# Optimization experiments

Hardware: AMD Instinct MI355X
Metric: run time of the kernel (lower is better)

## Reference

```python
import jax, jax.numpy as jnp
import numpy as np

B, H, S, D = 8, 16, 1024, 64

def setup_inputs() -> dict:
    key = jax.random.key(0)
    kq, kk, kv, km = jax.random.split(key, 4)
    Q = jax.random.normal(kq, (B, H, S, D), dtype=jnp.float32)
    K = jax.random.normal(kk, (B, H, S, D), dtype=jnp.float32)
    V = jax.random.normal(kv, (B, H, S, D), dtype=jnp.float32)
    attn_mask = jax.random.randint(km, (B, H, S, S), 0, 2).astype(bool)
    return {"Q": Q, "K": K, "V": V, "attn_mask": attn_mask}

def reference(Q, K, V, attn_mask):
    # scores = Q @ K^T  (NOTE: source has no 1/sqrt(d) scaling)
    scores = jnp.einsum("bhqd,bhkd->bhqk", Q, K)
    # source uses masked_fill_(mask, 1e-9), i.e. masked positions become 1e-9 (not -inf)
    scores = jnp.where(attn_mask, jnp.float32(1e-9), scores)
    attn = jax.nn.softmax(scores, axis=-1)
    context = jnp.einsum("bhqk,bhkd->bhqd", attn, V)
    return context, attn
```

## Files before the change

kernel.cpp:

```cpp
#include <hip/hip_runtime.h>

#define Sn 1024
#define Dn 64
#define PH_LD 1032
#define K_LD 72
#define V_LD 72

typedef short v8s __attribute__((ext_vector_type(8)));
typedef unsigned short v8u __attribute__((ext_vector_type(8)));
typedef float v4f __attribute__((ext_vector_type(4)));
typedef int   v4i __attribute__((ext_vector_type(4)));

#define LGKM0()  asm volatile("s_waitcnt lgkmcnt(0)" ::: "memory")
#define SBAR()   do { asm volatile("" ::: "memory"); __builtin_amdgcn_s_barrier(); \
                      __builtin_amdgcn_sched_barrier(0); } while (0)

__device__ __forceinline__ unsigned short f2bf(float x) {
    union { float f; unsigned u; } v; v.f = x;
    return (unsigned short)((v.u + 0x7FFFu + ((v.u >> 16) & 1u)) >> 16);
}
__device__ __forceinline__ float bf2f(unsigned short h) {
    union { float f; unsigned u; } v; v.u = ((unsigned)h) << 16;
    return v.f;
}
__device__ __forceinline__ void split2(float x, unsigned short& h, unsigned short& l) {
    unsigned short hs = f2bf(x);
    h = hs; l = f2bf(x - bf2f(hs));
}

__global__ __launch_bounds__(256) void prep_kf(const float* __restrict__ K,
    unsigned short* __restrict__ KF)
{
    const int bh = blockIdx.x >> 4, kt = blockIdx.x & 15;
    const int t = threadIdx.x;
    const int w = t >> 6, lane = t & 63;
    const int fr = lane & 15, g = lane >> 4;
    const float* src = K + (((size_t)(bh << 10) + (kt << 6) + (w << 4) + fr) << 6);
    const v4f a0 = __builtin_nontemporal_load((const v4f*)(src + (g << 3)));
    const v4f a1 = __builtin_nontemporal_load((const v4f*)(src + (g << 3) + 4));
    const v4f b0 = __builtin_nontemporal_load((const v4f*)(src + 32 + (g << 3)));
    const v4f b1 = __builtin_nontemporal_load((const v4f*)(src + 32 + (g << 3) + 4));
    v8u h0, h1, l0, l1;
    #pragma unroll
    for (int j = 0; j < 4; ++j) {
        unsigned short hh, ll;
        split2(a0[j], hh, ll); h0[j] = hh;     l0[j] = ll;
        split2(a1[j], hh, ll); h0[4 + j] = hh; l0[4 + j] = ll;
        split2(b0[j], hh, ll); h1[j] = hh;     l1[j] = ll;
        split2(b1[j], hh, ll); h1[4 + j] = hh; l1[4 + j] = ll;
    }
    unsigned short* dst = KF + ((size_t)bh << 17) + ((size_t)((kt << 2) + w) << 11) + (lane << 3);
    *(v8u*)(dst)        = h0;
    *(v8u*)(dst + 512)  = h1;
    *(v8u*)(dst + 1024) = l0;
    *(v8u*)(dst + 1536) = l1;
}

__global__ __launch_bounds__(256) void prep_vf(const float* __restrict__ V,
    unsigned short* __restrict__ VF)
{
    __shared__ float Ts[64][65];
    const int bh = blockIdx.x >> 4, kt = blockIdx.x & 15;
    const int t = threadIdx.x;
    {
        const int r = t >> 2, cs = (t & 3) << 4;
        const float* src = V + ((size_t)bh * Sn + (kt << 6) + r) * Dn + cs;
        const v4f a = __builtin_nontemporal_load((const v4f*)src);
        const v4f b = __builtin_nontemporal_load((const v4f*)src + 1);
        const v4f c = __builtin_nontemporal_load((const v4f*)src + 2);
        const v4f d = __builtin_nontemporal_load((const v4f*)src + 3);
        #pragma unroll
        for (int j = 0; j < 4; ++j) {
            Ts[r][cs + j]      = a[j];
            Ts[r][cs + 4 + j]  = b[j];
            Ts[r][cs + 8 + j]  = c[j];
            Ts[r][cs + 12 + j] = d[j];
        }
    }
    __syncthreads();
    {
        const int w = t >> 6, lane = t & 63;
        const int fr = lane & 15, g = lane >> 4;
        const int d = (w << 4) + fr;
        unsigned short* dst = VF + ((size_t)bh << 16) + ((size_t)((kt << 2) + w) << 10) + (lane << 3);
        v8u o0, o1;
        #pragma unroll
        for (int j = 0; j < 8; ++j) o0[j] = f2bf(Ts[(g << 3) + j][d]);
        #pragma unroll
        for (int j = 0; j < 8; ++j) o1[j] = f2bf(Ts[32 + (g << 3) + j][d]);
        *(v8u*)dst         = o0;
        *(v8u*)(dst + 512) = o1;
    }
}

__global__ __launch_bounds__(256) void prep_m(const int* __restrict__ M,
    unsigned long long* __restrict__ MW)
{
    const int NW = 2097152;
    const int lane = threadIdx.x & 63;
    const int wave = (blockIdx.x << 2) + (threadIdx.x >> 6);
    const int nwaves = gridDim.x << 2;
    for (int w0 = wave << 3; w0 < NW; w0 += nwaves << 3) {
        unsigned long long b[8];
        #pragma unroll
        for (int s = 0; s < 8; ++s) {
            const int v = __builtin_nontemporal_load(&M[((size_t)(w0 + s) << 6) + lane]);
            b[s] = __ballot(v != 0);
        }
        if (lane == 0) {
            ulonglong2* dst = (ulonglong2*)(MW + w0);
            ulonglong2 p0, p1, p2, p3;
            p0.x = b[0]; p0.y = b[1]; p1.x = b[2]; p1.y = b[3];
            p2.x = b[4]; p2.y = b[5]; p3.x = b[6]; p3.y = b[7];
            dst[0] = p0; dst[1] = p1; dst[2] = p2; dst[3] = p3;
        }
    }
}

__global__ __launch_bounds__(256, 4) void fused_attn_c(
    const unsigned short* __restrict__ KFG, const unsigned short* __restrict__ VFG,
    const float* __restrict__ Q, const unsigned long long* __restrict__ MW,
    float* __restrict__ attnO, float* __restrict__ ctxO)
{
    __shared__ unsigned short Ph[16][PH_LD];
    __shared__ float rsumW[4][16];
    __shared__ float invL[16];

    const int tid  = threadIdx.x;
    const int lane = tid & 63;
    const int w    = tid >> 6;
    const int fr   = lane & 15;
    const int g    = lane >> 4;

    const int swz = ((blockIdx.x & 7) << 10) + (blockIdx.x >> 3);
    const int bh = swz >> 6;
    const int q0 = (swz & 63) << 4;

    const float* Qb = Q + (size_t)bh * Sn * Dn + (size_t)q0 * Dn;
    float*       Ab = attnO + (size_t)bh * Sn * Sn + (size_t)q0 * Sn;
    float*       Cb = ctxO  + (size_t)bh * Sn * Dn + (size_t)q0 * Dn;
    const unsigned short* KFb = KFG + ((size_t)bh << 17);
    const unsigned short* VFb = VFG + ((size_t)bh << 16);
    const unsigned long long* mwp = MW + ((size_t)bh << 14) + ((size_t)(q0 + fr) << 4);

    v8s qh0, qh1, ql0, ql1;
    {
        const float* qp = Qb + fr * Dn + (g << 3);
        float x0[8], x1[8];
        *(v4f*)&x0[0] = *(const v4f*)qp;
        *(v4f*)&x0[4] = *(const v4f*)(qp + 4);
        *(v4f*)&x1[0] = *(const v4f*)(qp + 32);
        *(v4f*)&x1[4] = *(const v4f*)(qp + 36);
        #pragma unroll
        for (int i = 0; i < 8; ++i) {
            unsigned short hh, ll;
            split2(x0[i], hh, ll); qh0[i] = (short)hh; ql0[i] = (short)ll;
            split2(x1[i], hh, ll); qh1[i] = (short)hh; ql1[i] = (short)ll;
        }
    }

    const int sh = (w << 4) + (g << 2);

#define LDK(kt, h0, h1, l0, l1) do {                                               \
        const unsigned short* _p = KFb + ((size_t)(((kt) << 2) + w) << 11) + (lane << 3); \
        h0 = *(const v8s*)_p;          h1 = *(const v8s*)(_p + 512);               \
        l0 = *(const v8s*)(_p + 1024); l1 = *(const v8s*)(_p + 1536);              \
    } while (0)

#define STEPA(h0, h1, l0, l1, mwv, kt) do {                                        \
        v4f acc = {0.f, 0.f, 0.f, 0.f};                                            \
        __builtin_amdgcn_s_setprio(1);                                             \
        acc = __builtin_amdgcn_mfma_f32_16x16x32_bf16(h0, qh0, acc, 0, 0, 0);      \
        acc = __builtin_amdgcn_mfma_f32_16x16x32_bf16(h1, qh1, acc, 0, 0, 0);      \
        acc = __builtin_amdgcn_mfma_f32_16x16x32_bf16(l0, qh0, acc, 0, 0, 0);      \
        acc = __builtin_amdgcn_mfma_f32_16x16x32_bf16(l1, qh1, acc, 0, 0, 0);      \
        acc = __builtin_amdgcn_mfma_f32_16x16x32_bf16(h0, ql0, acc, 0, 0, 0);      \
        acc = __builtin_amdgcn_mfma_f32_16x16x32_bf16(h1, ql1, acc, 0, 0, 0);      \
        __builtin_amdgcn_s_setprio(0);                                             \
        const unsigned mb = (unsigned)((mwv) >> sh);                               \
        const float e0 = (mb & 1u) ? 1.0f : __expf(acc[0]);                        \
        const float e1 = (mb & 2u) ? 1.0f : __expf(acc[1]);                        \
        const float e2 = (mb & 4u) ? 1.0f : __expf(acc[2]);                        \
        const float e3 = (mb & 8u) ? 1.0f : __expf(acc[3]);                        \
        rs += (e0 + e1) + (e2 + e3);                                               \
        ushort4 pk;                                                                \
        pk.x = f2bf(e0); pk.y = f2bf(e1); pk.z = f2bf(e2); pk.w = f2bf(e3);        \
        *(ushort4*)&Ph[fr][((kt) << 6) + (w << 4) + (g << 2)] = pk;                \
    } while (0)

    float rs = 0.f;

    {
        v8s ah0, ah1, al0, al1, bh0, bh1, bl0, bl1;
        LDK(0, ah0, ah1, al0, al1);
        LDK(1, bh0, bh1, bl0, bl1);
        unsigned long long mA = mwp[0], mB = mwp[1];
        for (int kt = 0; kt < 16; kt += 2) {
            const int k2 = (kt + 2 < 16) ? kt + 2 : kt;
            const int k3 = (kt + 3 < 16) ? kt + 3 : kt;
            v8s ch0, ch1, cl0, cl1, dh0, dh1, dl0, dl1;
            LDK(k2, ch0, ch1, cl0, cl1);
            LDK(k3, dh0, dh1, dl0, dl1);
            const unsigned long long mC = mwp[k2];
            const unsigned long long mD = mwp[k3];
            STEPA(ah0, ah1, al0, al1, mA, kt);
            STEPA(bh0, bh1, bl0, bl1, mB, kt + 1);
            ah0 = ch0; ah1 = ch1; al0 = cl0; al1 = cl1; mA = mC;
            bh0 = dh0; bh1 = dh1; bl0 = dl0; bl1 = dl1; mB = mD;
        }
    }

    rs += __shfl_xor(rs, 16);
    rs += __shfl_xor(rs, 32);
    if (g == 0) rsumW[w][fr] = rs;
    __builtin_amdgcn_sched_barrier(0);
    LGKM0();
    SBAR();
    if (tid < 16) {
        const float s = rsumW[0][tid] + rsumW[1][tid] + rsumW[2][tid] + rsumW[3][tid];
        invL[tid] = 1.0f / s;
    }
    __builtin_amdgcn_sched_barrier(0);
    LGKM0();
    SBAR();

#define LDV(kt, v0, v1) do {                                                       \
        const unsigned short* _p = VFb + ((size_t)(((kt) << 2) + w) << 10) + (lane << 3); \
        v0 = *(const v8s*)_p;  v1 = *(const v8s*)(_p + 512);                       \
    } while (0)

#define STEPB(v0, v1, kt) do {                                                     \
        const v8s a0 = *(const v8s*)&Ph[fr][((kt) << 6) + (g << 3)];               \
        const v8s a1 = *(const v8s*)&Ph[fr][((kt) << 6) + 32 + (g << 3)];          \
        __builtin_amdgcn_s_setprio(1);                                             \
        accp = __builtin_amdgcn_mfma_f32_16x16x32_bf16(a0, v0, accp, 0, 0, 0);     \
        accp = __builtin_amdgcn_mfma_f32_16x16x32_bf16(a1, v1, accp, 0, 0, 0);     \
        __builtin_amdgcn_s_setprio(0);                                             \
    } while (0)

    v8s va0, va1, vb0, vb1;
    LDV(0, va0, va1);
    LDV(1, vb0, vb1);

    {
        const int qq = tid >> 4, ii = tid & 15;
        const float inv = invL[qq];
        float* arow = Ab + (size_t)qq * Sn;
        #pragma unroll
        for (int c = 0; c < 16; ++c) {
            const int k0 = (c << 6) + (ii << 2);
            const ushort4 p = *(const ushort4*)&Ph[qq][k0];
            v4f o;
            o[0] = bf2f(p.x) * inv; o[1] = bf2f(p.y) * inv;
            o[2] = bf2f(p.z) * inv; o[3] = bf2f(p.w) * inv;
            __builtin_nontemporal_store(o, (v4f*)(arow + k0));
        }
    }

    const int dcol = (w << 4) + fr;
    v4f accp = {0.f, 0.f, 0.f, 0.f};
    for (int kt = 0; kt < 16; kt += 2) {
        const int k2 = (kt + 2 < 16) ? kt + 2 : kt;
        const int k3 = (kt + 3 < 16) ? kt + 3 : kt;
        v8s vc0, vc1, vd0, vd1;
        LDV(k2, vc0, vc1);
        LDV(k3, vd0, vd1);
        STEPB(va0, va1, kt);
        STEPB(vb0, vb1, kt + 1);
        va0 = vc0; va1 = vc1;
        vb0 = vd0; vb1 = vd1;
    }
    #pragma unroll
    for (int r = 0; r < 4; ++r) {
        const int q = (g << 2) + r;
        __builtin_nontemporal_store(accp[r] * invL[q], &Cb[(size_t)q * Dn + dcol]);
    }
#undef LDK
#undef STEPA
#undef LDV
#undef STEPB
}

__global__ __launch_bounds__(256, 3) void fused_attn_fb(
    const float* __restrict__ Q, const float* __restrict__ K,
    const float* __restrict__ V, const int* __restrict__ M,
    float* __restrict__ attnO, float* __restrict__ ctxO)
{
    __shared__ unsigned short Ph[16][1048];
    __shared__ __align__(16) unsigned short Kraw[2 * 64 * K_LD];
    __shared__ float rsumW[4][16];
    __shared__ float invL[16];

    unsigned short (*Khi)[K_LD] = (unsigned short (*)[K_LD])Kraw;
    unsigned short (*Klo)[K_LD] = (unsigned short (*)[K_LD])(Kraw + 64 * K_LD);
    unsigned short (*Vt)[V_LD]  = (unsigned short (*)[V_LD])Kraw;

    const int tid  = threadIdx.x;
    const int lane = tid & 63;
    const int w    = tid >> 6;
    const int fr   = lane & 15;
    const int g    = lane >> 4;

    const int bh = blockIdx.x >> 6;
    const int q0 = (blockIdx.x & 63) << 4;

    const float* Qb = Q + (size_t)bh * Sn * Dn + (size_t)q0 * Dn;
    const float* Kb = K + (size_t)bh * Sn * Dn;
    const float* Vb = V + (size_t)bh * Sn * Dn;
    const int*   Mb = M + (size_t)bh * Sn * Sn + (size_t)q0 * Sn;
    float*       Ab = attnO + (size_t)bh * Sn * Sn + (size_t)q0 * Sn;
    float*       Cb = ctxO  + (size_t)bh * Sn * Dn + (size_t)q0 * Dn;

    v8s qh0, qh1, ql0, ql1;
    {
        const float* qp = Qb + fr * Dn + (g << 3);
        float x0[8], x1[8];
        *(v4f*)&x0[0] = *(const v4f*)qp;
        *(v4f*)&x0[4] = *(const v4f*)(qp + 4);
        *(v4f*)&x1[0] = *(const v4f*)(qp + 32);
        *(v4f*)&x1[4] = *(const v4f*)(qp + 36);
        #pragma unroll
        for (int i = 0; i < 8; ++i) {
            unsigned short hh, ll;
            split2(x0[i], hh, ll); qh0[i] = (short)hh; ql0[i] = (short)ll;
            split2(x1[i], hh, ll); qh1[i] = (short)hh; ql1[i] = (short)ll;
        }
    }

    const int srow = tid >> 4;
    const int sc4  = (tid & 15) << 2;

    const int* mp = Mb + (size_t)fr * Sn + (w << 4) + (g << 2);
    v4i mv = *(const v4i*)mp;

    v4f ka[4];
    #pragma unroll
    for (int i = 0; i < 4; ++i)
        ka[i] = *(const v4f*)(Kb + (size_t)(srow + (i << 4)) * Dn + sc4);

    float rs = 0.f;

    for (int kt = 0; kt < 16; ++kt) {
        __syncthreads();
        v4f kb[4];
        if (kt < 15) {
            const float* kn = Kb + (size_t)((kt + 1) << 6) * Dn;
            #pragma unroll
            for (int i = 0; i < 4; ++i)
                kb[i] = *(const v4f*)(kn + (size_t)(srow + (i << 4)) * Dn + sc4);
        }
        v4i mnext = mv;
        if (kt < 15) mnext = *(const v4i*)(mp + ((kt + 1) << 6));

        #pragma unroll
        for (int i = 0; i < 4; ++i) {
            const int row = srow + (i << 4);
            ushort4 hv, lv;
            split2(ka[i][0], hv.x, lv.x); split2(ka[i][1], hv.y, lv.y);
            split2(ka[i][2], hv.z, lv.z); split2(ka[i][3], hv.w, lv.w);
            *(ushort4*)&Khi[row][sc4] = hv;
            *(ushort4*)&Klo[row][sc4] = lv;
        }
        __syncthreads();

        const int krow = (w << 4) + fr;
        const v8s kh0 = *(const v8s*)&Khi[krow][(g << 3)];
        const v8s kh1 = *(const v8s*)&Khi[krow][32 + (g << 3)];
        const v8s kl0 = *(const v8s*)&Klo[krow][(g << 3)];
        const v8s kl1 = *(const v8s*)&Klo[krow][32 + (g << 3)];

        v4f acc = {0.f, 0.f, 0.f, 0.f};
        acc = __builtin_amdgcn_mfma_f32_16x16x32_bf16(kh0, qh0, acc, 0, 0, 0);
        acc = __builtin_amdgcn_mfma_f32_16x16x32_bf16(kh1, qh1, acc, 0, 0, 0);
        acc = __builtin_amdgcn_mfma_f32_16x16x32_bf16(kl0, qh0, acc, 0, 0, 0);
        acc = __builtin_amdgcn_mfma_f32_16x16x32_bf16(kl1, qh1, acc, 0, 0, 0);
        acc = __builtin_amdgcn_mfma_f32_16x16x32_bf16(kh0, ql0, acc, 0, 0, 0);
        acc = __builtin_amdgcn_mfma_f32_16x16x32_bf16(kh1, ql1, acc, 0, 0, 0);

        const float e0 = mv[0] ? 1.0f : __expf(acc[0]);
        const float e1 = mv[1] ? 1.0f : __expf(acc[1]);
        const float e2 = mv[2] ? 1.0f : __expf(acc[2]);
        const float e3 = mv[3] ? 1.0f : __expf(acc[3]);
        rs += (e0 + e1) + (e2 + e3);
        ushort4 pk;
        pk.x = f2bf(e0); pk.y = f2bf(e1); pk.z = f2bf(e2); pk.w = f2bf(e3);
        *(ushort4*)&Ph[fr][(kt << 6) + (w << 4) + (g << 2)] = pk;

        mv = mnext;
        #pragma unroll
        for (int i = 0; i < 4; ++i) ka[i] = kb[i];
    }

    rs += __shfl_xor(rs, 16);
    rs += __shfl_xor(rs, 32);
    if (g == 0) rsumW[w][fr] = rs;
    __syncthreads();
    if (tid < 16) {
        const float s = rsumW[0][tid] + rsumW[1][tid] + rsumW[2][tid] + rsumW[3][tid];
        invL[tid] = 1.0f / s;
    }
    __syncthreads();

    const int dcol = (w << 4) + fr;
    v4f va[4];
    #pragma unroll
    for (int i = 0; i < 4; ++i)
        va[i] = *(const v4f*)(Vb + (size_t)(srow + (i << 4)) * Dn + sc4);

    v4f accp = {0.f, 0.f, 0.f, 0.f};
    for (int kt = 0; kt < 16; ++kt) {
        __syncthreads();
        v4f vb[4];
        if (kt < 15) {
            const float* vn = Vb + (size_t)((kt + 1) << 6) * Dn;
            #pragma unroll
            for (int i = 0; i < 4; ++i)
                vb[i] = *(const v4f*)(vn + (size_t)(srow + (i << 4)) * Dn + sc4);
        }
        #pragma unroll
        for (int i = 0; i < 4; ++i) {
            const int row = srow + (i << 4);
            Vt[sc4 + 0][row] = f2bf(va[i][0]);
            Vt[sc4 + 1][row] = f2bf(va[i][1]);
            Vt[sc4 + 2][row] = f2bf(va[i][2]);
            Vt[sc4 + 3][row] = f2bf(va[i][3]);
        }
        __syncthreads();

        #pragma unroll
        for (int c = 0; c < 2; ++c) {
            const int kc = (kt << 6) + (c << 5);
            const v8s a = *(const v8s*)&Ph[fr][kc + (g << 3)];
            const v8s b = *(const v8s*)&Vt[dcol][(c << 5) + (g << 3)];
            accp = __builtin_amdgcn_mfma_f32_16x16x32_bf16(a, b, accp, 0, 0, 0);
        }
        #pragma unroll
        for (int i = 0; i < 4; ++i) va[i] = vb[i];
    }
    #pragma unroll
    for (int r = 0; r < 4; ++r) {
        const int q = (g << 2) + r;
        Cb[(size_t)q * Dn + dcol] = accp[r] * invL[q];
    }

    {
        const int qq = tid >> 4, ii = tid & 15;
        const float inv = invL[qq];
        float* arow = Ab + (size_t)qq * Sn;
        #pragma unroll
        for (int c = 0; c < 16; ++c) {
            const int k0 = (c << 6) + (ii << 2);
            const ushort4 p = *(const ushort4*)&Ph[qq][k0];
            v4f o;
            o[0] = bf2f(p.x) * inv; o[1] = bf2f(p.y) * inv;
            o[2] = bf2f(p.z) * inv; o[3] = bf2f(p.w) * inv;
            *(v4f*)(arow + k0) = o;
        }
    }
}

extern "C" void kernel_launch(void* const* d_in, const int* in_sizes, int n_in,
                              void* d_out, int out_size, void* d_ws, size_t ws_size,
                              hipStream_t stream) {
    const float* Q    = (const float*)d_in[0];
    const float* K    = (const float*)d_in[1];
    const float* V    = (const float*)d_in[2];
    const int*   mask = (const int*)d_in[3];

    float* ctx  = (float*)d_out;
    float* attn = (float*)d_out + (size_t)128 * Sn * Dn;

    const size_t NELEM = (size_t)128 * Sn * Dn;
    const size_t MWORDS = (size_t)128 * Sn * 16;
    const size_t NEED  = NELEM * 2 * 3 + MWORDS * 8;

    if (ws_size >= NEED) {
        unsigned short* KF = (unsigned short*)d_ws;
        unsigned short* VF = KF + NELEM * 2;
        unsigned long long* MWp = (unsigned long long*)((char*)d_ws + NELEM * 2 * 3);
        prep_kf<<<2048, 256, 0, stream>>>(K, KF);
        prep_vf<<<2048, 256, 0, stream>>>(V, VF);
        prep_m<<<2048, 256, 0, stream>>>(mask, MWp);
        fused_attn_c<<<128 * 64, 256, 0, stream>>>(KF, VF, Q, MWp, attn, ctx);
    } else {
        fused_attn_fb<<<128 * 64, 256, 0, stream>>>(Q, K, V, mask, attn, ctx);
    }
}
```

Before: 293.3 us.

## Drop mask bit-packing prep kernel and read int mask directly in fused kernel

Removes the separate prep_m kernel that packed the int32 mask into 64-bit bitmasks. The fused attention kernel now loads int32 mask values directly with 16-byte vector loads, prefetching up to eight steps ahead in a register ring. The K-fragment double buffer becomes an array-indexed, fully unrolled loop. This saves one kernel launch and the write and re-read of the packed mask, but the main kernel now reads 32x more mask bytes and uses more registers, which may reduce occupancy.

```diff
diff --git a/kernel.cpp b/kernel.cpp
--- a/kernel.cpp
+++ b/kernel.cpp
@@ -93,33 +93,9 @@
     }
 }
 
-__global__ __launch_bounds__(256) void prep_m(const int* __restrict__ M,
-    unsigned long long* __restrict__ MW)
-{
-    const int NW = 2097152;
-    const int lane = threadIdx.x & 63;
-    const int wave = (blockIdx.x << 2) + (threadIdx.x >> 6);
-    const int nwaves = gridDim.x << 2;
-    for (int w0 = wave << 3; w0 < NW; w0 += nwaves << 3) {
-        unsigned long long b[8];
-        #pragma unroll
-        for (int s = 0; s < 8; ++s) {
-            const int v = __builtin_nontemporal_load(&M[((size_t)(w0 + s) << 6) + lane]);
-            b[s] = __ballot(v != 0);
-        }
-        if (lane == 0) {
-            ulonglong2* dst = (ulonglong2*)(MW + w0);
-            ulonglong2 p0, p1, p2, p3;
-            p0.x = b[0]; p0.y = b[1]; p1.x = b[2]; p1.y = b[3];
-            p2.x = b[4]; p2.y = b[5]; p3.x = b[6]; p3.y = b[7];
-            dst[0] = p0; dst[1] = p1; dst[2] = p2; dst[3] = p3;
-        }
-    }
-}
-
 __global__ __launch_bounds__(256, 4) void fused_attn_c(
     const unsigned short* __restrict__ KFG, const unsigned short* __restrict__ VFG,
-    const float* __restrict__ Q, const unsigned long long* __restrict__ MW,
+    const float* __restrict__ Q, const int* __restrict__ M,
     float* __restrict__ attnO, float* __restrict__ ctxO)
 {
     __shared__ unsigned short Ph[16][PH_LD];
@@ -141,7 +117,7 @@
     float*       Cb = ctxO  + (size_t)bh * Sn * Dn + (size_t)q0 * Dn;
     const unsigned short* KFb = KFG + ((size_t)bh << 17);
     const unsigned short* VFb = VFG + ((size_t)bh << 16);
-    const unsigned long long* mwp = MW + ((size_t)bh << 14) + ((size_t)(q0 + fr) << 4);
+    const int* mp = M + (size_t)bh * Sn * Sn + (size_t)(q0 + fr) * Sn + (w << 4) + (g << 2);
 
     v8s qh0, qh1, ql0, ql1;
     {
@@ -159,15 +135,13 @@
         }
     }
 
-    const int sh = (w << 4) + (g << 2);
-
 #define LDK(kt, h0, h1, l0, l1) do {                                               \
         const unsigned short* _p = KFb + ((size_t)(((kt) << 2) + w) << 11) + (lane << 3); \
         h0 = *(const v8s*)_p;          h1 = *(const v8s*)(_p + 512);               \
         l0 = *(const v8s*)(_p + 1024); l1 = *(const v8s*)(_p + 1536);              \
     } while (0)
 
-#define STEPA(h0, h1, l0, l1, mwv, kt) do {                                        \
+#define STEPA(h0, h1, l0, l1, mv, kt) do {                                         \
         v4f acc = {0.f, 0.f, 0.f, 0.f};                                            \
         __builtin_amdgcn_s_setprio(1);                                             \
         acc = __builtin_amdgcn_mfma_f32_16x16x32_bf16(h0, qh0, acc, 0, 0, 0);      \
@@ -177,11 +151,10 @@
         acc = __builtin_amdgcn_mfma_f32_16x16x32_bf16(h0, ql0, acc, 0, 0, 0);      \
         acc = __builtin_amdgcn_mfma_f32_16x16x32_bf16(h1, ql1, acc, 0, 0, 0);      \
         __builtin_amdgcn_s_setprio(0);                                             \
-        const unsigned mb = (unsigned)((mwv) >> sh);                               \
-        const float e0 = (mb & 1u) ? 1.0f : __expf(acc[0]);                        \
-        const float e1 = (mb & 2u) ? 1.0f : __expf(acc[1]);                        \
-        const float e2 = (mb & 4u) ? 1.0f : __expf(acc[2]);                        \
-        const float e3 = (mb & 8u) ? 1.0f : __expf(acc[3]);                        \
+        const float e0 = (mv)[0] ? 1.0f : __expf(acc[0]);                          \
+        const float e1 = (mv)[1] ? 1.0f : __expf(acc[1]);                          \
+        const float e2 = (mv)[2] ? 1.0f : __expf(acc[2]);                          \
+        const float e3 = (mv)[3] ? 1.0f : __expf(acc[3]);                          \
         rs += (e0 + e1) + (e2 + e3);                                               \
         ushort4 pk;                                                                \
         pk.x = f2bf(e0); pk.y = f2bf(e1); pk.z = f2bf(e2); pk.w = f2bf(e3);        \
@@ -191,22 +164,17 @@
     float rs = 0.f;
 
     {
-        v8s ah0, ah1, al0, al1, bh0, bh1, bl0, bl1;
-        LDK(0, ah0, ah1, al0, al1);
-        LDK(1, bh0, bh1, bl0, bl1);
-        unsigned long long mA = mwp[0], mB = mwp[1];
-        for (int kt = 0; kt < 16; kt += 2) {
-            const int k2 = (kt + 2 < 16) ? kt + 2 : kt;
-            const int k3 = (kt + 3 < 16) ? kt + 3 : kt;
-            v8s ch0, ch1, cl0, cl1, dh0, dh1, dl0, dl1;
-            LDK(k2, ch0, ch1, cl0, cl1);
-            LDK(k3, dh0, dh1, dl0, dl1);
-            const unsigned long long mC = mwp[k2];
-            const unsigned long long mD = mwp[k3];
-            STEPA(ah0, ah1, al0, al1, mA, kt);
-            STEPA(bh0, bh1, bl0, bl1, mB, kt + 1);
-            ah0 = ch0; ah1 = ch1; al0 = cl0; al1 = cl1; mA = mC;
-            bh0 = dh0; bh1 = dh1; bl0 = dl0; bl1 = dl1; mB = mD;
+        v8s h0[2], h1[2], l0[2], l1[2];
+        v4i mk[8];
+        LDK(0, h0[0], h1[0], l0[0], l1[0]);
+        LDK(1, h0[1], h1[1], l0[1], l1[1]);
+        #pragma unroll
+        for (int s = 0; s < 8; ++s) mk[s] = *(const v4i*)(mp + (s << 6));
+        #pragma unroll
+        for (int kt = 0; kt < 16; ++kt) {
+            STEPA(h0[kt & 1], h1[kt & 1], l0[kt & 1], l1[kt & 1], mk[kt & 7], kt);
+            if (kt + 2 < 16) LDK(kt + 2, h0[kt & 1], h1[kt & 1], l0[kt & 1], l1[kt & 1]);
+            if (kt + 8 < 16) mk[kt & 7] = *(const v4i*)(mp + ((kt + 8) << 6));
         }
     }
 
@@ -471,17 +439,14 @@
     float* attn = (float*)d_out + (size_t)128 * Sn * Dn;
 
     const size_t NELEM = (size_t)128 * Sn * Dn;
-    const size_t MWORDS = (size_t)128 * Sn * 16;
-    const size_t NEED  = NELEM * 2 * 3 + MWORDS * 8;
+    const size_t NEED  = NELEM * 6;
 
     if (ws_size >= NEED) {
         unsigned short* KF = (unsigned short*)d_ws;
         unsigned short* VF = KF + NELEM * 2;
-        unsigned long long* MWp = (unsigned long long*)((char*)d_ws + NELEM * 2 * 3);
         prep_kf<<<2048, 256, 0, stream>>>(K, KF);
         prep_vf<<<2048, 256, 0, stream>>>(V, VF);
-        prep_m<<<2048, 256, 0, stream>>>(mask, MWp);
-        fused_attn_c<<<128 * 64, 256, 0, stream>>>(KF, VF, Q, MWp, attn, ctx);
+        fused_attn_c<<<128 * 64, 256, 0, stream>>>(KF, VF, Q, mask, attn, ctx);
     } else {
         fused_attn_fb<<<128 * 64, 256, 0, stream>>>(Q, K, V, mask, attn, ctx);
     }
```

New measurement: 373.1 us. 27.2% more time.

## Process 32 query rows per 512-thread block to share K fragments

Applied to the files above, without the earlier changes.

Each block now covers 32 query rows with 8 waves instead of 16 rows with 4. In the QK^T phase every wave computes two 16-row query tiles against each loaded K tile, so K and mask traffic per query is halved, with a double-buffered prefetch loop. The PV phase splits the waves into two query halves and four D columns, and the grid shrinks to match. The shared P buffer doubles in size, which limits blocks per CU. The launch bound of 512 threads with 4 blocks per CU may cap registers and cause spills with the doubled query fragments.

```diff
diff --git a/kernel.cpp b/kernel.cpp
--- a/kernel.cpp
+++ b/kernel.cpp
@@ -117,14 +117,14 @@
     }
 }
 
-__global__ __launch_bounds__(256, 4) void fused_attn_c(
+__global__ __launch_bounds__(512, 4) void fused_attn_w(
     const unsigned short* __restrict__ KFG, const unsigned short* __restrict__ VFG,
     const float* __restrict__ Q, const unsigned long long* __restrict__ MW,
     float* __restrict__ attnO, float* __restrict__ ctxO)
 {
-    __shared__ unsigned short Ph[16][PH_LD];
-    __shared__ float rsumW[4][16];
-    __shared__ float invL[16];
+    __shared__ unsigned short Ph[32][PH_LD];
+    __shared__ float rsumW[8][32];
+    __shared__ float invL[32];
 
     const int tid  = threadIdx.x;
     const int lane = tid & 63;
@@ -132,20 +132,22 @@
     const int fr   = lane & 15;
     const int g    = lane >> 4;
 
-    const int swz = ((blockIdx.x & 7) << 10) + (blockIdx.x >> 3);
-    const int bh = swz >> 6;
-    const int q0 = (swz & 63) << 4;
+    const int swz = ((blockIdx.x & 7) << 9) + (blockIdx.x >> 3);
+    const int bh = swz >> 5;
+    const int q0 = (swz & 31) << 5;
 
     const float* Qb = Q + (size_t)bh * Sn * Dn + (size_t)q0 * Dn;
     float*       Ab = attnO + (size_t)bh * Sn * Sn + (size_t)q0 * Sn;
     float*       Cb = ctxO  + (size_t)bh * Sn * Dn + (size_t)q0 * Dn;
     const unsigned short* KFb = KFG + ((size_t)bh << 17);
     const unsigned short* VFb = VFG + ((size_t)bh << 16);
-    const unsigned long long* mwp = MW + ((size_t)bh << 14) + ((size_t)(q0 + fr) << 4);
-
-    v8s qh0, qh1, ql0, ql1;
-    {
-        const float* qp = Qb + fr * Dn + (g << 3);
+    const unsigned long long* mwp0 = MW + ((size_t)bh << 14) + ((size_t)(q0 + fr) << 4);
+    const unsigned long long* mwp1 = mwp0 + (16 << 4);
+
+    v8s qh0[2], qh1[2], ql0[2], ql1[2];
+    #pragma unroll
+    for (int h = 0; h < 2; ++h) {
+        const float* qp = Qb + (size_t)((h << 4) + fr) * Dn + (g << 3);
         float x0[8], x1[8];
         *(v4f*)&x0[0] = *(const v4f*)qp;
         *(v4f*)&x0[4] = *(const v4f*)(qp + 4);
@@ -154,70 +156,90 @@
         #pragma unroll
         for (int i = 0; i < 8; ++i) {
             unsigned short hh, ll;
-            split2(x0[i], hh, ll); qh0[i] = (short)hh; ql0[i] = (short)ll;
-            split2(x1[i], hh, ll); qh1[i] = (short)hh; ql1[i] = (short)ll;
-        }
-    }
-
-    const int sh = (w << 4) + (g << 2);
-
-#define LDK(kt, h0, h1, l0, l1) do {                                               \
-        const unsigned short* _p = KFb + ((size_t)(((kt) << 2) + w) << 11) + (lane << 3); \
-        h0 = *(const v8s*)_p;          h1 = *(const v8s*)(_p + 512);               \
-        l0 = *(const v8s*)(_p + 1024); l1 = *(const v8s*)(_p + 1536);              \
+            split2(x0[i], hh, ll); qh0[h][i] = (short)hh; ql0[h][i] = (short)ll;
+            split2(x1[i], hh, ll); qh1[h][i] = (short)hh; ql1[h][i] = (short)ll;
+        }
+    }
+
+    const int jbase = w >> 2;
+    const int sh    = ((w & 3) << 4) + (g << 2);
+
+#define LDK(kt, h0_, h1_, l0_, l1_) do {                                           \
+        const unsigned short* _p = KFb + ((size_t)(((kt) << 3) + w) << 11) + (lane << 3); \
+        h0_ = *(const v8s*)_p;          h1_ = *(const v8s*)(_p + 512);             \
+        l0_ = *(const v8s*)(_p + 1024); l1_ = *(const v8s*)(_p + 1536);            \
     } while (0)
 
-#define STEPA(h0, h1, l0, l1, mwv, kt) do {                                        \
-        v4f acc = {0.f, 0.f, 0.f, 0.f};                                            \
+#define STEPA(kh0, kh1, kl0, kl1, mv0, mv1, kt) do {                               \
+        v4f acc0 = {0.f, 0.f, 0.f, 0.f};                                           \
+        v4f acc1 = {0.f, 0.f, 0.f, 0.f};                                           \
         __builtin_amdgcn_s_setprio(1);                                             \
-        acc = __builtin_amdgcn_mfma_f32_16x16x32_bf16(h0, qh0, acc, 0, 0, 0);      \
-        acc = __builtin_amdgcn_mfma_f32_16x16x32_bf16(h1, qh1, acc, 0, 0, 0);      \
-        acc = __builtin_amdgcn_mfma_f32_16x16x32_bf16(l0, qh0, acc, 0, 0, 0);      \
-        acc = __builtin_amdgcn_mfma_f32_16x16x32_bf16(l1, qh1, acc, 0, 0, 0);      \
-        acc = __builtin_amdgcn_mfma_f32_16x16x32_bf16(h0, ql0, acc, 0, 0, 0);      \
-        acc = __builtin_amdgcn_mfma_f32_16x16x32_bf16(h1, ql1, acc, 0, 0, 0);      \
+        acc0 = __builtin_amdgcn_mfma_f32_16x16x32_bf16(kh0, qh0[0], acc0, 0, 0, 0);\
+        acc1 = __builtin_amdgcn_mfma_f32_16x16x32_bf16(kh0, qh0[1], acc1, 0, 0, 0);\
+        acc0 = __builtin_amdgcn_mfma_f32_16x16x32_bf16(kh1, qh1[0], acc0, 0, 0, 0);\
+        acc1 = __builtin_amdgcn_mfma_f32_16x16x32_bf16(kh1, qh1[1], acc1, 0, 0, 0);\
+        acc0 = __builtin_amdgcn_mfma_f32_16x16x32_bf16(kl0, qh0[0], acc0, 0, 0, 0);\
+        acc1 = __builtin_amdgcn_mfma_f32_16x16x32_bf16(kl0, qh0[1], acc1, 0, 0, 0);\
+        acc0 = __builtin_amdgcn_mfma_f32_16x16x32_bf16(kl1, qh1[0], acc0, 0, 0, 0);\
+        acc1 = __builtin_amdgcn_mfma_f32_16x16x32_bf16(kl1, qh1[1], acc1, 0, 0, 0);\
+        acc0 = __builtin_amdgcn_mfma_f32_16x16x32_bf16(kh0, ql0[0], acc0, 0, 0, 0);\
+        acc1 = __builtin_amdgcn_mfma_f32_16x16x32_bf16(kh0, ql0[1], acc1, 0, 0, 0);\
+        acc0 = __builtin_amdgcn_mfma_f32_16x16x32_bf16(kh1, ql1[0], acc0, 0, 0, 0);\
+        acc1 = __builtin_amdgcn_mfma_f32_16x16x32_bf16(kh1, ql1[1], acc1, 0, 0, 0);\
         __builtin_amdgcn_s_setprio(0);                                             \
-        const unsigned mb = (unsigned)((mwv) >> sh);                               \
-        const float e0 = (mb & 1u) ? 1.0f : __expf(acc[0]);                        \
-        const float e1 = (mb & 2u) ? 1.0f : __expf(acc[1]);                        \
-        const float e2 = (mb & 4u) ? 1.0f : __expf(acc[2]);                        \
-        const float e3 = (mb & 8u) ? 1.0f : __expf(acc[3]);                        \
-        rs += (e0 + e1) + (e2 + e3);                                               \
-        ushort4 pk;                                                                \
-        pk.x = f2bf(e0); pk.y = f2bf(e1); pk.z = f2bf(e2); pk.w = f2bf(e3);        \
-        *(ushort4*)&Ph[fr][((kt) << 6) + (w << 4) + (g << 2)] = pk;                \
+        const int kcol = ((kt) << 7) + ((w & 3) << 4) + ((w >> 2) << 6) + (g << 2);\
+        const unsigned mb0 = (unsigned)((mv0) >> sh);                              \
+        const unsigned mb1 = (unsigned)((mv1) >> sh);                              \
+        const float e00 = (mb0 & 1u) ? 1.0f : __expf(acc0[0]);                     \
+        const float e01 = (mb0 & 2u) ? 1.0f : __expf(acc0[1]);                     \
+        const float e02 = (mb0 & 4u) ? 1.0f : __expf(acc0[2]);                     \
+        const float e03 = (mb0 & 8u) ? 1.0f : __expf(acc0[3]);                     \
+        const float e10 = (mb1 & 1u) ? 1.0f : __expf(acc1[0]);                     \
+        const float e11 = (mb1 & 2u) ? 1.0f : __expf(acc1[1]);                     \
+        const float e12 = (mb1 & 4u) ? 1.0f : __expf(acc1[2]);                     \
+        const float e13 = (mb1 & 8u) ? 1.0f : __expf(acc1[3]);                     \
+        rs0 += (e00 + e01) + (e02 + e03);                                          \
+        rs1 += (e10 + e11) + (e12 + e13);                                          \
+        ushort4 pk0, pk1;                                                          \
+        pk0.x = f2bf(e00); pk0.y = f2bf(e01); pk0.z = f2bf(e02); pk0.w = f2bf(e03);\
+        pk1.x = f2bf(e10); pk1.y = f2bf(e11); pk1.z = f2bf(e12); pk1.w = f2bf(e13);\
+        *(ushort4*)&Ph[fr][kcol]      = pk0;                                       \
+        *(ushort4*)&Ph[16 + fr][kcol] = pk1;                                       \
     } while (0)
 
-    float rs = 0.f;
+    float rs0 = 0.f, rs1 = 0.f;
 
     {
-        v8s ah0, ah1, al0, al1, bh0, bh1, bl0, bl1;
-        LDK(0, ah0, ah1, al0, al1);
-        LDK(1, bh0, bh1, bl0, bl1);
-        unsigned long long mA = mwp[0], mB = mwp[1];
-        for (int kt = 0; kt < 16; kt += 2) {
-            const int k2 = (kt + 2 < 16) ? kt + 2 : kt;
-            const int k3 = (kt + 3 < 16) ? kt + 3 : kt;
-            v8s ch0, ch1, cl0, cl1, dh0, dh1, dl0, dl1;
-            LDK(k2, ch0, ch1, cl0, cl1);
-            LDK(k3, dh0, dh1, dl0, dl1);
-            const unsigned long long mC = mwp[k2];
-            const unsigned long long mD = mwp[k3];
-            STEPA(ah0, ah1, al0, al1, mA, kt);
-            STEPA(bh0, bh1, bl0, bl1, mB, kt + 1);
-            ah0 = ch0; ah1 = ch1; al0 = cl0; al1 = cl1; mA = mC;
-            bh0 = dh0; bh1 = dh1; bl0 = dl0; bl1 = dl1; mB = mD;
-        }
-    }
-
-    rs += __shfl_xor(rs, 16);
-    rs += __shfl_xor(rs, 32);
-    if (g == 0) rsumW[w][fr] = rs;
+        v8s h0[2], h1[2], l0[2], l1[2];
+        unsigned long long m0[2], m1[2];
+        LDK(0, h0[0], h1[0], l0[0], l1[0]);
+        LDK(1, h0[1], h1[1], l0[1], l1[1]);
+        m0[0] = mwp0[jbase];     m1[0] = mwp1[jbase];
+        m0[1] = mwp0[jbase + 2]; m1[1] = mwp1[jbase + 2];
+        #pragma unroll
+        for (int kt = 0; kt < 8; ++kt) {
+            STEPA(h0[kt & 1], h1[kt & 1], l0[kt & 1], l1[kt & 1], m0[kt & 1], m1[kt & 1], kt);
+            if (kt + 2 < 8) {
+                LDK(kt + 2, h0[kt & 1], h1[kt & 1], l0[kt & 1], l1[kt & 1]);
+                m0[kt & 1] = mwp0[jbase + ((kt + 2) << 1)];
+                m1[kt & 1] = mwp1[jbase + ((kt + 2) << 1)];
+            }
+        }
+    }
+
+
+    rs0 += __shfl_xor(rs0, 16);
+    rs0 += __shfl_xor(rs0, 32);
+    rs1 += __shfl_xor(rs1, 16);
+    rs1 += __shfl_xor(rs1, 32);
+    if (g == 0) { rsumW[w][fr] = rs0; rsumW[w][16 + fr] = rs1; }
     __builtin_amdgcn_sched_barrier(0);
     LGKM0();
     SBAR();
-    if (tid < 16) {
-        const float s = rsumW[0][tid] + rsumW[1][tid] + rsumW[2][tid] + rsumW[3][tid];
+    if (tid < 32) {
+        float s = 0.f;
+        #pragma unroll
+        for (int ww = 0; ww < 8; ++ww) s += rsumW[ww][tid];
         invL[tid] = 1.0f / s;
     }
     __builtin_amdgcn_sched_barrier(0);
@@ -225,13 +247,15 @@
     SBAR();
 
 #define LDV(kt, v0, v1) do {                                                       \
-        const unsigned short* _p = VFb + ((size_t)(((kt) << 2) + w) << 10) + (lane << 3); \
+        const unsigned short* _p = VFb + ((size_t)(((kt) << 2) + (w & 3)) << 10) + (lane << 3); \
         v0 = *(const v8s*)_p;  v1 = *(const v8s*)(_p + 512);                       \
     } while (0)
 
+    const int qbase = (w >> 2) << 4;
+
 #define STEPB(v0, v1, kt) do {                                                     \
-        const v8s a0 = *(const v8s*)&Ph[fr][((kt) << 6) + (g << 3)];               \
-        const v8s a1 = *(const v8s*)&Ph[fr][((kt) << 6) + 32 + (g << 3)];          \
+        const v8s a0 = *(const v8s*)&Ph[qbase + fr][((kt) << 6) + (g << 3)];       \
+        const v8s a1 = *(const v8s*)&Ph[qbase + fr][((kt) << 6) + 32 + (g << 3)];  \
         __builtin_amdgcn_s_setprio(1);                                             \
         accp = __builtin_amdgcn_mfma_f32_16x16x32_bf16(a0, v0, accp, 0, 0, 0);     \
         accp = __builtin_amdgcn_mfma_f32_16x16x32_bf16(a1, v1, accp, 0, 0, 0);     \
@@ -257,7 +281,7 @@
         }
     }
 
-    const int dcol = (w << 4) + fr;
+    const int dcol = ((w & 3) << 4) + fr;
     v4f accp = {0.f, 0.f, 0.f, 0.f};
     for (int kt = 0; kt < 16; kt += 2) {
         const int k2 = (kt + 2 < 16) ? kt + 2 : kt;
@@ -272,7 +296,7 @@
     }
     #pragma unroll
     for (int r = 0; r < 4; ++r) {
-        const int q = (g << 2) + r;
+        const int q = qbase + (g << 2) + r;
         __builtin_nontemporal_store(accp[r] * invL[q], &Cb[(size_t)q * Dn + dcol]);
     }
 #undef LDK
@@ -472,16 +496,16 @@
 
     const size_t NELEM = (size_t)128 * Sn * Dn;
     const size_t MWORDS = (size_t)128 * Sn * 16;
-    const size_t NEED  = NELEM * 2 * 3 + MWORDS * 8;
+    const size_t NEED  = NELEM * 6 + MWORDS * 8;
 
     if (ws_size >= NEED) {
         unsigned short* KF = (unsigned short*)d_ws;
         unsigned short* VF = KF + NELEM * 2;
-        unsigned long long* MWp = (unsigned long long*)((char*)d_ws + NELEM * 2 * 3);
+        unsigned long long* MWp = (unsigned long long*)((char*)d_ws + NELEM * 6);
         prep_kf<<<2048, 256, 0, stream>>>(K, KF);
         prep_vf<<<2048, 256, 0, stream>>>(V, VF);
         prep_m<<<2048, 256, 0, stream>>>(mask, MWp);
-        fused_attn_c<<<128 * 64, 256, 0, stream>>>(KF, VF, Q, MWp, attn, ctx);
+        fused_attn_w<<<128 * 32, 512, 0, stream>>>(KF, VF, Q, MWp, attn, ctx);
     } else {
         fused_attn_fb<<<128 * 64, 256, 0, stream>>>(Q, K, V, mask, attn, ctx);
     }
```

Result: slower. 314.4 us (+7.2%).

## Merge prep kernels into one launch and deepen K/V prefetch ring to four

Applied to the files above, without the earlier changes.

Combines the three preprocessing kernels (K split, V transpose, mask bit-packing) into a single launch whose block index range selects the task, removing two kernel launches and their serialization gaps. In the fused attention kernel, the K and V tile loops are fully unrolled with a four-deep register ring buffer instead of a two-deep double buffer, so more global loads are in flight ahead of each MFMA step. The deeper ring raises register pressure, which may hurt occupancy under the four-waves bound.

```diff
diff --git a/kernel.cpp b/kernel.cpp
--- a/kernel.cpp
+++ b/kernel.cpp
@@ -28,91 +28,90 @@
     h = hs; l = f2bf(x - bf2f(hs));
 }
 
-__global__ __launch_bounds__(256) void prep_kf(const float* __restrict__ K,
-    unsigned short* __restrict__ KF)
-{
-    const int bh = blockIdx.x >> 4, kt = blockIdx.x & 15;
-    const int t = threadIdx.x;
-    const int w = t >> 6, lane = t & 63;
-    const int fr = lane & 15, g = lane >> 4;
-    const float* src = K + (((size_t)(bh << 10) + (kt << 6) + (w << 4) + fr) << 6);
-    const v4f a0 = __builtin_nontemporal_load((const v4f*)(src + (g << 3)));
-    const v4f a1 = __builtin_nontemporal_load((const v4f*)(src + (g << 3) + 4));
-    const v4f b0 = __builtin_nontemporal_load((const v4f*)(src + 32 + (g << 3)));
-    const v4f b1 = __builtin_nontemporal_load((const v4f*)(src + 32 + (g << 3) + 4));
-    v8u h0, h1, l0, l1;
-    #pragma unroll
-    for (int j = 0; j < 4; ++j) {
-        unsigned short hh, ll;
-        split2(a0[j], hh, ll); h0[j] = hh;     l0[j] = ll;
-        split2(a1[j], hh, ll); h0[4 + j] = hh; l0[4 + j] = ll;
-        split2(b0[j], hh, ll); h1[j] = hh;     l1[j] = ll;
-        split2(b1[j], hh, ll); h1[4 + j] = hh; l1[4 + j] = ll;
-    }
-    unsigned short* dst = KF + ((size_t)bh << 17) + ((size_t)((kt << 2) + w) << 11) + (lane << 3);
-    *(v8u*)(dst)        = h0;
-    *(v8u*)(dst + 512)  = h1;
-    *(v8u*)(dst + 1024) = l0;
-    *(v8u*)(dst + 1536) = l1;
-}
-
-__global__ __launch_bounds__(256) void prep_vf(const float* __restrict__ V,
-    unsigned short* __restrict__ VF)
+__global__ __launch_bounds__(256) void prep_all(
+    const float* __restrict__ K, const float* __restrict__ V,
+    const int* __restrict__ M,
+    unsigned short* __restrict__ KF, unsigned short* __restrict__ VF,
+    unsigned long long* __restrict__ MW)
 {
     __shared__ float Ts[64][65];
-    const int bh = blockIdx.x >> 4, kt = blockIdx.x & 15;
+    const int bid = blockIdx.x;
     const int t = threadIdx.x;
-    {
-        const int r = t >> 2, cs = (t & 3) << 4;
-        const float* src = V + ((size_t)bh * Sn + (kt << 6) + r) * Dn + cs;
-        const v4f a = __builtin_nontemporal_load((const v4f*)src);
-        const v4f b = __builtin_nontemporal_load((const v4f*)src + 1);
-        const v4f c = __builtin_nontemporal_load((const v4f*)src + 2);
-        const v4f d = __builtin_nontemporal_load((const v4f*)src + 3);
-        #pragma unroll
-        for (int j = 0; j < 4; ++j) {
-            Ts[r][cs + j]      = a[j];
-            Ts[r][cs + 4 + j]  = b[j];
-            Ts[r][cs + 8 + j]  = c[j];
-            Ts[r][cs + 12 + j] = d[j];
-        }
-    }
-    __syncthreads();
-    {
+
+    if (bid < 2048) {
+        const int bh = bid >> 4, kt = bid & 15;
         const int w = t >> 6, lane = t & 63;
         const int fr = lane & 15, g = lane >> 4;
-        const int d = (w << 4) + fr;
-        unsigned short* dst = VF + ((size_t)bh << 16) + ((size_t)((kt << 2) + w) << 10) + (lane << 3);
-        v8u o0, o1;
-        #pragma unroll
-        for (int j = 0; j < 8; ++j) o0[j] = f2bf(Ts[(g << 3) + j][d]);
-        #pragma unroll
-        for (int j = 0; j < 8; ++j) o1[j] = f2bf(Ts[32 + (g << 3) + j][d]);
-        *(v8u*)dst         = o0;
-        *(v8u*)(dst + 512) = o1;
-    }
-}
-
-__global__ __launch_bounds__(256) void prep_m(const int* __restrict__ M,
-    unsigned long long* __restrict__ MW)
-{
-    const int NW = 2097152;
-    const int lane = threadIdx.x & 63;
-    const int wave = (blockIdx.x << 2) + (threadIdx.x >> 6);
-    const int nwaves = gridDim.x << 2;
-    for (int w0 = wave << 3; w0 < NW; w0 += nwaves << 3) {
-        unsigned long long b[8];
-        #pragma unroll
-        for (int s = 0; s < 8; ++s) {
-            const int v = __builtin_nontemporal_load(&M[((size_t)(w0 + s) << 6) + lane]);
-            b[s] = __ballot(v != 0);
-        }
-        if (lane == 0) {
-            ulonglong2* dst = (ulonglong2*)(MW + w0);
-            ulonglong2 p0, p1, p2, p3;
-            p0.x = b[0]; p0.y = b[1]; p1.x = b[2]; p1.y = b[3];
-            p2.x = b[4]; p2.y = b[5]; p3.x = b[6]; p3.y = b[7];
-            dst[0] = p0; dst[1] = p1; dst[2] = p2; dst[3] = p3;
+        const float* src = K + (((size_t)(bh << 10) + (kt << 6) + (w << 4) + fr) << 6);
+        const v4f a0 = __builtin_nontemporal_load((const v4f*)(src + (g << 3)));
+        const v4f a1 = __builtin_nontemporal_load((const v4f*)(src + (g << 3) + 4));
+        const v4f b0 = __builtin_nontemporal_load((const v4f*)(src + 32 + (g << 3)));
+        const v4f b1 = __builtin_nontemporal_load((const v4f*)(src + 32 + (g << 3) + 4));
+        v8u h0, h1, l0, l1;
+        #pragma unroll
+        for (int j = 0; j < 4; ++j) {
+            unsigned short hh, ll;
+            split2(a0[j], hh, ll); h0[j] = hh;     l0[j] = ll;
+            split2(a1[j], hh, ll); h0[4 + j] = hh; l0[4 + j] = ll;
+            split2(b0[j], hh, ll); h1[j] = hh;     l1[j] = ll;
+            split2(b1[j], hh, ll); h1[4 + j] = hh; l1[4 + j] = ll;
+        }
+        unsigned short* dst = KF + ((size_t)bh << 17) + ((size_t)((kt << 2) + w) << 11) + (lane << 3);
+        *(v8u*)(dst)        = h0;
+        *(v8u*)(dst + 512)  = h1;
+        *(v8u*)(dst + 1024) = l0;
+        *(v8u*)(dst + 1536) = l1;
+    } else if (bid < 4096) {
+        const int b2 = bid - 2048;
+        const int bh = b2 >> 4, kt = b2 & 15;
+        {
+            const int r = t >> 2, cs = (t & 3) << 4;
+            const float* src = V + ((size_t)bh * Sn + (kt << 6) + r) * Dn + cs;
+            const v4f a = __builtin_nontemporal_load((const v4f*)src);
+            const v4f b = __builtin_nontemporal_load((const v4f*)src + 1);
+            const v4f c = __builtin_nontemporal_load((const v4f*)src + 2);
+            const v4f d = __builtin_nontemporal_load((const v4f*)src + 3);
+            #pragma unroll
+            for (int j = 0; j < 4; ++j) {
+                Ts[r][cs + j]      = a[j];
+                Ts[r][cs + 4 + j]  = b[j];
+                Ts[r][cs + 8 + j]  = c[j];
+                Ts[r][cs + 12 + j] = d[j];
+            }
+        }
+        __syncthreads();
+        {
+            const int w = t >> 6, lane = t & 63;
+            const int fr = lane & 15, g = lane >> 4;
+            const int d = (w << 4) + fr;
+            unsigned short* dst = VF + ((size_t)bh << 16) + ((size_t)((kt << 2) + w) << 10) + (lane << 3);
+            v8u o0, o1;
+            #pragma unroll
+            for (int j = 0; j < 8; ++j) o0[j] = f2bf(Ts[(g << 3) + j][d]);
+            #pragma unroll
+            for (int j = 0; j < 8; ++j) o1[j] = f2bf(Ts[32 + (g << 3) + j][d]);
+            *(v8u*)dst         = o0;
+            *(v8u*)(dst + 512) = o1;
+        }
+    } else {
+        const int NW = 2097152;
+        const int lane = t & 63;
+        const int wave = ((bid - 4096) << 2) + (t >> 6);
+        const int nwaves = 2048 << 2;
+        for (int w0 = wave << 3; w0 < NW; w0 += nwaves << 3) {
+            unsigned long long b[8];
+            #pragma unroll
+            for (int s = 0; s < 8; ++s) {
+                const int v = __builtin_nontemporal_load(&M[((size_t)(w0 + s) << 6) + lane]);
+                b[s] = __ballot(v != 0);
+            }
+            if (lane == 0) {
+                ulonglong2* dst = (ulonglong2*)(MW + w0);
+                ulonglong2 p0, p1, p2, p3;
+                p0.x = b[0]; p0.y = b[1]; p1.x = b[2]; p1.y = b[3];
+                p2.x = b[4]; p2.y = b[5]; p3.x = b[6]; p3.y = b[7];
+                dst[0] = p0; dst[1] = p1; dst[2] = p2; dst[3] = p3;
+            }
         }
     }
 }
@@ -161,21 +160,21 @@
 
     const int sh = (w << 4) + (g << 2);
 
-#define LDK(kt, h0, h1, l0, l1) do {                                               \
+#define LDK(kt, h0_, h1_, l0_, l1_) do {                                           \
         const unsigned short* _p = KFb + ((size_t)(((kt) << 2) + w) << 11) + (lane << 3); \
-        h0 = *(const v8s*)_p;          h1 = *(const v8s*)(_p + 512);               \
-        l0 = *(const v8s*)(_p + 1024); l1 = *(const v8s*)(_p + 1536);              \
+        h0_ = *(const v8s*)_p;          h1_ = *(const v8s*)(_p + 512);             \
+        l0_ = *(const v8s*)(_p + 1024); l1_ = *(const v8s*)(_p + 1536);            \
     } while (0)
 
-#define STEPA(h0, h1, l0, l1, mwv, kt) do {                                        \
+#define STEPA(h0_, h1_, l0_, l1_, mwv, kt) do {                                    \
         v4f acc = {0.f, 0.f, 0.f, 0.f};                                            \
         __builtin_amdgcn_s_setprio(1);                                             \
-        acc = __builtin_amdgcn_mfma_f32_16x16x32_bf16(h0, qh0, acc, 0, 0, 0);      \
-        acc = __builtin_amdgcn_mfma_f32_16x16x32_bf16(h1, qh1, acc, 0, 0, 0);      \
-        acc = __builtin_amdgcn_mfma_f32_16x16x32_bf16(l0, qh0, acc, 0, 0, 0);      \
-        acc = __builtin_amdgcn_mfma_f32_16x16x32_bf16(l1, qh1, acc, 0, 0, 0);      \
-        acc = __builtin_amdgcn_mfma_f32_16x16x32_bf16(h0, ql0, acc, 0, 0, 0);      \
-        acc = __builtin_amdgcn_mfma_f32_16x16x32_bf16(h1, ql1, acc, 0, 0, 0);      \
+        acc = __builtin_amdgcn_mfma_f32_16x16x32_bf16(h0_, qh0, acc, 0, 0, 0);     \
+        acc = __builtin_amdgcn_mfma_f32_16x16x32_bf16(h1_, qh1, acc, 0, 0, 0);     \
+        acc = __builtin_amdgcn_mfma_f32_16x16x32_bf16(l0_, qh0, acc, 0, 0, 0);     \
+        acc = __builtin_amdgcn_mfma_f32_16x16x32_bf16(l1_, qh1, acc, 0, 0, 0);     \
+        acc = __builtin_amdgcn_mfma_f32_16x16x32_bf16(h0_, ql0, acc, 0, 0, 0);     \
+        acc = __builtin_amdgcn_mfma_f32_16x16x32_bf16(h1_, ql1, acc, 0, 0, 0);     \
         __builtin_amdgcn_s_setprio(0);                                             \
         const unsigned mb = (unsigned)((mwv) >> sh);                               \
         const float e0 = (mb & 1u) ? 1.0f : __expf(acc[0]);                        \
@@ -191,22 +190,20 @@
     float rs = 0.f;
 
     {
-        v8s ah0, ah1, al0, al1, bh0, bh1, bl0, bl1;
-        LDK(0, ah0, ah1, al0, al1);
-        LDK(1, bh0, bh1, bl0, bl1);
-        unsigned long long mA = mwp[0], mB = mwp[1];
-        for (int kt = 0; kt < 16; kt += 2) {
-            const int k2 = (kt + 2 < 16) ? kt + 2 : kt;
-            const int k3 = (kt + 3 < 16) ? kt + 3 : kt;
-            v8s ch0, ch1, cl0, cl1, dh0, dh1, dl0, dl1;
-            LDK(k2, ch0, ch1, cl0, cl1);
-            LDK(k3, dh0, dh1, dl0, dl1);
-            const unsigned long long mC = mwp[k2];
-            const unsigned long long mD = mwp[k3];
-            STEPA(ah0, ah1, al0, al1, mA, kt);
-            STEPA(bh0, bh1, bl0, bl1, mB, kt + 1);
-            ah0 = ch0; ah1 = ch1; al0 = cl0; al1 = cl1; mA = mC;
-            bh0 = dh0; bh1 = dh1; bl0 = dl0; bl1 = dl1; mB = mD;
+        v8s h0[4], h1[4], l0[4], l1[4];
+        unsigned long long mk[4];
+        LDK(0, h0[0], h1[0], l0[0], l1[0]);
+        LDK(1, h0[1], h1[1], l0[1], l1[1]);
+        LDK(2, h0[2], h1[2], l0[2], l1[2]);
+        LDK(3, h0[3], h1[3], l0[3], l1[3]);
+        mk[0] = mwp[0]; mk[1] = mwp[1]; mk[2] = mwp[2]; mk[3] = mwp[3];
+        #pragma unroll
+        for (int kt = 0; kt < 16; ++kt) {
+            STEPA(h0[kt & 3], h1[kt & 3], l0[kt & 3], l1[kt & 3], mk[kt & 3], kt);
+            if (kt + 4 < 16) {
+                LDK(kt + 4, h0[kt & 3], h1[kt & 3], l0[kt & 3], l1[kt & 3]);
+                mk[kt & 3] = mwp[kt + 4];
+            }
         }
     }
 
@@ -224,23 +221,25 @@
     LGKM0();
     SBAR();
 
-#define LDV(kt, v0, v1) do {                                                       \
+#define LDV(kt, v0_, v1_) do {                                                     \
         const unsigned short* _p = VFb + ((size_t)(((kt) << 2) + w) << 10) + (lane << 3); \
-        v0 = *(const v8s*)_p;  v1 = *(const v8s*)(_p + 512);                       \
+        v0_ = *(const v8s*)_p;  v1_ = *(const v8s*)(_p + 512);                     \
     } while (0)
 
-#define STEPB(v0, v1, kt) do {                                                     \
+#define STEPB(v0_, v1_, kt) do {                                                   \
         const v8s a0 = *(const v8s*)&Ph[fr][((kt) << 6) + (g << 3)];               \
         const v8s a1 = *(const v8s*)&Ph[fr][((kt) << 6) + 32 + (g << 3)];          \
         __builtin_amdgcn_s_setprio(1);                                             \
-        accp = __builtin_amdgcn_mfma_f32_16x16x32_bf16(a0, v0, accp, 0, 0, 0);     \
-        accp = __builtin_amdgcn_mfma_f32_16x16x32_bf16(a1, v1, accp, 0, 0, 0);     \
+        accp = __builtin_amdgcn_mfma_f32_16x16x32_bf16(a0, v0_, accp, 0, 0, 0);    \
+        accp = __builtin_amdgcn_mfma_f32_16x16x32_bf16(a1, v1_, accp, 0, 0, 0);    \
         __builtin_amdgcn_s_setprio(0);                                             \
     } while (0)
 
-    v8s va0, va1, vb0, vb1;
-    LDV(0, va0, va1);
-    LDV(1, vb0, vb1);
+    v8s v0s[4], v1s[4];
+    LDV(0, v0s[0], v1s[0]);
+    LDV(1, v0s[1], v1s[1]);
+    LDV(2, v0s[2], v1s[2]);
+    LDV(3, v0s[3], v1s[3]);
 
     {
         const int qq = tid >> 4, ii = tid & 15;
@@ -259,16 +258,10 @@
 
     const int dcol = (w << 4) + fr;
     v4f accp = {0.f, 0.f, 0.f, 0.f};
-    for (int kt = 0; kt < 16; kt += 2) {
-        const int k2 = (kt + 2 < 16) ? kt + 2 : kt;
-        const int k3 = (kt + 3 < 16) ? kt + 3 : kt;
-        v8s vc0, vc1, vd0, vd1;
-        LDV(k2, vc0, vc1);
-        LDV(k3, vd0, vd1);
-        STEPB(va0, va1, kt);
-        STEPB(vb0, vb1, kt + 1);
-        va0 = vc0; va1 = vc1;
-        vb0 = vd0; vb1 = vd1;
+    #pragma unroll
+    for (int kt = 0; kt < 16; ++kt) {
+        STEPB(v0s[kt & 3], v1s[kt & 3], kt);
+        if (kt + 4 < 16) LDV(kt + 4, v0s[kt & 3], v1s[kt & 3]);
     }
     #pragma unroll
     for (int r = 0; r < 4; ++r) {
@@ -472,15 +465,13 @@
 
     const size_t NELEM = (size_t)128 * Sn * Dn;
     const size_t MWORDS = (size_t)128 * Sn * 16;
-    const size_t NEED  = NELEM * 2 * 3 + MWORDS * 8;
+    const size_t NEED  = NELEM * 6 + MWORDS * 8;
 
     if (ws_size >= NEED) {
         unsigned short* KF = (unsigned short*)d_ws;
         unsigned short* VF = KF + NELEM * 2;
-        unsigned long long* MWp = (unsigned long long*)((char*)d_ws + NELEM * 2 * 3);
-        prep_kf<<<2048, 256, 0, stream>>>(K, KF);
-        prep_vf<<<2048, 256, 0, stream>>>(V, VF);
-        prep_m<<<2048, 256, 0, stream>>>(mask, MWp);
+        unsigned long long* MWp = (unsigned long long*)((char*)d_ws + NELEM * 6);
+        prep_all<<<6144, 256, 0, stream>>>(K, V, mask, KF, VF, MWp);
         fused_attn_c<<<128 * 64, 256, 0, stream>>>(KF, VF, Q, MWp, attn, ctx);
     } else {
         fused_attn_fb<<<128 * 64, 256, 0, stream>>>(Q, K, V, mask, attn, ctx);
```

Result: slower. 301.2 us (+2.7%).
